# Kernel optimization log

Hardware: AMD Instinct MI355X
Metric: run time of the kernel (lower is better)

## Reference

```python
import jax, jax.numpy as jnp
import numpy as np

D_MODEL = 1024
N_HEADS = 16
D_K = D_MODEL // N_HEADS


def setup_inputs() -> dict:
    key = jax.random.key(0)
    ks = jax.random.split(key, 5)
    s = 1.0 / np.sqrt(D_MODEL)
    x = jax.random.normal(ks[0], (4, 2048, D_MODEL), dtype=jnp.float32)
    W_qkv = jax.random.normal(ks[1], (D_MODEL, 3 * D_MODEL), dtype=jnp.float32) * s
    b_qkv = jnp.zeros((3 * D_MODEL,), dtype=jnp.float32)
    W_proj = jax.random.normal(ks[2], (D_MODEL, D_MODEL), dtype=jnp.float32) * s
    b_proj = jnp.zeros((D_MODEL,), dtype=jnp.float32)
    return {"x": x, "W_qkv": W_qkv, "b_qkv": b_qkv, "W_proj": W_proj, "b_proj": b_proj}


def reference(x, W_qkv, b_qkv, W_proj, b_proj):
    B, T, C = x.shape
    qkv = x @ W_qkv + b_qkv  # [B,T,3C]
    q, k, v = jnp.split(qkv, 3, axis=2)
    # [B,T,C] -> [B,H,T,dk]
    def to_heads(t):
        return t.reshape(B, T, N_HEADS, D_K).transpose(0, 2, 1, 3)
    q, k, v = to_heads(q), to_heads(k), to_heads(v)
    scale = 1.0 / np.sqrt(D_K)
    att = jnp.einsum('bhqd,bhkd->bhqk', q, k) * scale
    causal = jnp.tril(jnp.ones((T, T), dtype=bool))
    att = jnp.where(causal, att, -jnp.inf)
    att = jax.nn.softmax(att, axis=-1)
    y = jnp.einsum('bhqk,bhkd->bhqd', att, v)
    y = y.transpose(0, 2, 1, 3).reshape(B, T, C)
    return y @ W_proj + b_proj
```

## Files before the change

### kernel.cpp

```cpp
#include <hip/hip_runtime.h>
#include <stdint.h>


typedef float  floatx4 __attribute__((ext_vector_type(4)));
typedef __bf16 bf16x8  __attribute__((ext_vector_type(8)));
typedef __bf16 bf16x4  __attribute__((ext_vector_type(4)));

#define AS1 __attribute__((address_space(1)))
#define AS3 __attribute__((address_space(3)))

__device__ __forceinline__ void gload_lds16(const void* g, void* l) {
    __builtin_amdgcn_global_load_lds((AS1 void*)(uintptr_t)g,
                                     (AS3 void*)(uintptr_t)l, 16, 0, 0);
}

#if __has_builtin(__builtin_amdgcn_exp2f)
#define EXP2F(x) __builtin_amdgcn_exp2f(x)
#else
#define EXP2F(x) exp2f(x)
#endif

#define LOG2E 1.44269504088896340736f
#define ATT_SC (0.125f * LOG2E)
#define MASK_NEG (-3.0e4f)

static constexpr int Bn = 4, Tn = 2048, Cn = 1024, Hn = 16, DKn = 64;
static constexpr int BT = Bn * Tn;
static constexpr int N_QKV = 3 * Cn;
static constexpr int PAD = 68;
static constexpr int VPAD = 132;


__global__ void cast_x_kernel(const float* __restrict__ x, __bf16* __restrict__ xb, int n) {
    int i = (blockIdx.x * blockDim.x + threadIdx.x) * 4;
    if (i < n) {
        float4 v = *(const float4*)(x + i);
        bf16x4 o;
        o[0] = (__bf16)v.x; o[1] = (__bf16)v.y; o[2] = (__bf16)v.z; o[3] = (__bf16)v.w;
        *(bf16x4*)(xb + i) = o;
    }
}

__global__ void transpose_cast_kernel(const float* __restrict__ W, __bf16* __restrict__ WT,
                                      int R, int C) {
    __shared__ float tile[32][33];
    int tx = threadIdx.x & 31, ty = threadIdx.x >> 5;
    int r0 = blockIdx.y * 32, c0 = blockIdx.x * 32;
#pragma unroll
    for (int i = 0; i < 4; i++)
        tile[ty + i * 8][tx] = W[(size_t)(r0 + ty + i * 8) * C + c0 + tx];
    __syncthreads();
#pragma unroll
    for (int i = 0; i < 4; i++)
        WT[(size_t)(c0 + ty + i * 8) * R + r0 + tx] = (__bf16)tile[tx][ty + i * 8];
}

__device__ __forceinline__ void xcd_swizzle(int gx, int* bn, int* bm) {
    int flat = blockIdx.y * gx + blockIdx.x;
    int nwg = gx * gridDim.y;
    int cpx = nwg >> 3;
    int swz = (flat & 7) * cpx + (flat >> 3);
    *bm = swz / gx;
    *bn = swz - *bm * gx;
}

__global__ __launch_bounds__(256) void gemm_qkv_kernel(
    const __bf16* __restrict__ A, const __bf16* __restrict__ Bt,
    const float* __restrict__ bias,
    __bf16* __restrict__ Qo, __bf16* __restrict__ Ko, __bf16* __restrict__ Vo) {
    const int K = 1024;
    __shared__ __bf16 Al[128 * 64];
    __shared__ __bf16 Bl[128 * 64];
    int tid = threadIdx.x, w = tid >> 6, lane = tid & 63;
    int lq = lane >> 4, l16 = lane & 15;
    int bm, bn;
    xcd_swizzle(gridDim.x, &bn, &bm);
    int wm = w & 1, wn = w >> 1;

    int srow = lane >> 3;
    int scb  = (lane & 7) ^ (srow & 7);
    const __bf16* Ag = A + (size_t)(bm * 128 + w * 32 + srow) * K + scb * 8;
    const __bf16* Bg = Bt + (size_t)(bn * 128 + w * 32 + srow) * K + scb * 8;
    __bf16* AlW = Al + w * 32 * 64;
    __bf16* BlW = Bl + w * 32 * 64;

    const int co0 = ((0 * 4 + lq) ^ (l16 & 7)) * 8;
    const int co1 = ((1 * 4 + lq) ^ (l16 & 7)) * 8;

    floatx4 acc[4][4] = {};
    for (int k0 = 0; k0 < K; k0 += 64) {
        __syncthreads();
#pragma unroll
        for (int c = 0; c < 4; c++) {
            gload_lds16(Ag + k0 + (size_t)c * 8 * K, AlW + c * 8 * 64);
            gload_lds16(Bg + k0 + (size_t)c * 8 * K, BlW + c * 8 * 64);
        }
        __syncthreads();
#pragma unroll
        for (int ks = 0; ks < 2; ks++) {
            const int co = ks ? co1 : co0;
            bf16x8 af[4], bf[4];
#pragma unroll
            for (int i = 0; i < 4; i++)
                af[i] = *(const bf16x8*)&Al[(wm * 64 + i * 16 + l16) * 64 + co];
#pragma unroll
            for (int i = 0; i < 4; i++)
                bf[i] = *(const bf16x8*)&Bl[(wn * 64 + i * 16 + l16) * 64 + co];
#pragma unroll
            for (int mt = 0; mt < 4; mt++)
#pragma unroll
                for (int nt = 0; nt < 4; nt++)
                    acc[mt][nt] = __builtin_amdgcn_mfma_f32_16x16x32_bf16(
                        af[mt], bf[nt], acc[mt][nt], 0, 0, 0);
        }
    }
#pragma unroll
    for (int nt = 0; nt < 4; nt++) {
        int gbase = bn * 128 + wn * 64 + nt * 16;
        int gcol = gbase + l16;
        int which = gbase >> 10;
        float bv = bias[gcol];
        if (which == 2) {
            int hh = (gbase - 2048) >> 6;
            int dd = ((gbase - 2048) & 63) + l16;
#pragma unroll
            for (int mt = 0; mt < 4; mt++) {
                int growb = bm * 128 + wm * 64 + mt * 16 + lq * 4;
                int bb = growb >> 11, tt = growb & 2047;
                bf16x4 v4;
#pragma unroll
                for (int r = 0; r < 4; r++) v4[r] = (__bf16)(acc[mt][nt][r] + bv);
                *(bf16x4*)&Vo[((size_t)(bb * 16 + hh) * 64 + dd) * 2048 + tt] = v4;
            }
        } else {
            int rem = gbase & 1023;
            int hh = rem >> 6, dd = (rem & 63) + l16;
            __bf16* dst = (which == 0) ? Qo : Ko;
            float scl = (which == 0) ? ATT_SC : 1.0f;
#pragma unroll
            for (int mt = 0; mt < 4; mt++) {
#pragma unroll
                for (int r = 0; r < 4; r++) {
                    int grow = bm * 128 + wm * 64 + mt * 16 + lq * 4 + r;
                    int bb = grow >> 11, tt = grow & 2047;
                    dst[((size_t)(bb * 16 + hh) * 2048 + tt) * 64 + dd] =
                        (__bf16)((acc[mt][nt][r] + bv) * scl);
                }
            }
        }
    }
}

__global__ __launch_bounds__(256) void gemm_proj_kernel(
    const __bf16* __restrict__ A, const __bf16* __restrict__ Bt,
    const float* __restrict__ bias, float* __restrict__ out) {
    const int K = 1024;
    __shared__ __bf16 Al[128 * 64];
    __shared__ __bf16 Bl[128 * 64];
    int tid = threadIdx.x, w = tid >> 6, lane = tid & 63;
    int lq = lane >> 4, l16 = lane & 15;
    int bm, bn;
    xcd_swizzle(gridDim.x, &bn, &bm);
    int wm = w & 1, wn = w >> 1;

    int srow = lane >> 3;
    int scb  = (lane & 7) ^ (srow & 7);
    const __bf16* Ag = A + (size_t)(bm * 128 + w * 32 + srow) * K + scb * 8;
    const __bf16* Bg = Bt + (size_t)(bn * 128 + w * 32 + srow) * K + scb * 8;
    __bf16* AlW = Al + w * 32 * 64;
    __bf16* BlW = Bl + w * 32 * 64;

    const int co0 = ((0 * 4 + lq) ^ (l16 & 7)) * 8;
    const int co1 = ((1 * 4 + lq) ^ (l16 & 7)) * 8;

    floatx4 acc[4][4] = {};
    for (int k0 = 0; k0 < K; k0 += 64) {
        __syncthreads();
#pragma unroll
        for (int c = 0; c < 4; c++) {
            gload_lds16(Ag + k0 + (size_t)c * 8 * K, AlW + c * 8 * 64);
            gload_lds16(Bg + k0 + (size_t)c * 8 * K, BlW + c * 8 * 64);
        }
        __syncthreads();
#pragma unroll
        for (int ks = 0; ks < 2; ks++) {
            const int co = ks ? co1 : co0;
            bf16x8 af[4], bf[4];
#pragma unroll
            for (int i = 0; i < 4; i++)
                af[i] = *(const bf16x8*)&Al[(wm * 64 + i * 16 + l16) * 64 + co];
#pragma unroll
            for (int i = 0; i < 4; i++)
                bf[i] = *(const bf16x8*)&Bl[(wn * 64 + i * 16 + l16) * 64 + co];
#pragma unroll
            for (int mt = 0; mt < 4; mt++)
#pragma unroll
                for (int nt = 0; nt < 4; nt++)
                    acc[mt][nt] = __builtin_amdgcn_mfma_f32_16x16x32_bf16(
                        af[mt], bf[nt], acc[mt][nt], 0, 0, 0);
        }
    }
#pragma unroll
    for (int nt = 0; nt < 4; nt++) {
        int gcol = bn * 128 + wn * 64 + nt * 16 + l16;
        float bv = bias[gcol];
#pragma unroll
        for (int mt = 0; mt < 4; mt++) {
#pragma unroll
            for (int r = 0; r < 4; r++) {
                int grow = bm * 128 + wm * 64 + mt * 16 + lq * 4 + r;
                out[(size_t)grow * 1024 + gcol] = acc[mt][nt][r] + bv;
            }
        }
    }
}

__global__ __launch_bounds__(256) void attn_kernel(
    const __bf16* __restrict__ Q, const __bf16* __restrict__ K,
    const __bf16* __restrict__ Vt, __bf16* __restrict__ Y) {
    const int bid = blockIdx.x;
    const int pr = bid >> 6, bh = bid & 63;
    const int b = bh >> 4, h = bh & 15;
    int tid = threadIdx.x, w = tid >> 6, lane = tid & 63;
    int lq = lane >> 4, l16 = lane & 15;

    const __bf16* Qh = Q + (size_t)bh * Tn * DKn;
    const __bf16* Kh = K + (size_t)bh * Tn * DKn;
    const __bf16* Vh = Vt + (size_t)bh * DKn * Tn;

    __shared__ __bf16 Kl[128 * PAD];
    __shared__ __bf16 Vl[64 * VPAD];
    __shared__ __bf16 Pl[128 * PAD];

    int skrow = tid >> 3, sksl = tid & 7;
    int svrow = tid >> 4, svsl = tid & 15;

    bf16x8 onesf;
#pragma unroll
    for (int j = 0; j < 8; j++) onesf[j] = (__bf16)1.0f;

    bf16x8 kr[4], vr[4];
#pragma unroll
    for (int i = 0; i < 4; i++) {
        kr[i] = *(const bf16x8*)&Kh[(size_t)(skrow + i * 32) * 64 + sksl * 8];
        vr[i] = *(const bf16x8*)&Vh[(size_t)(svrow + i * 16) * 2048 + svsl * 8];
    }

#pragma unroll
    for (int seg = 0; seg < 2; seg++) {
        const int qt = seg ? (15 - pr) : pr;
        const int q0 = qt * 128;
        const int ktmax = qt;

        bf16x8 qf[2][2];
#pragma unroll
        for (int mt = 0; mt < 2; mt++)
#pragma unroll
            for (int ks = 0; ks < 2; ks++)
                qf[mt][ks] = *(const bf16x8*)&Qh[(size_t)(q0 + w * 32 + mt * 16 + l16) * 64 +
                                                 ks * 32 + lq * 8];

        floatx4 oacc[2][5] = {};

        for (int kt = 0; kt <= ktmax; kt++) {
            __syncthreads();
#pragma unroll
            for (int i = 0; i < 4; i++) {
                *(bf16x8*)&Kl[(skrow + i * 32) * PAD + sksl * 8] = kr[i];
                *(bf16x8*)&Vl[(svrow + i * 16) * VPAD + svsl * 8] = vr[i];
            }
            __syncthreads();
            if (!(seg == 1 && kt == ktmax)) {
                int nk = (kt < ktmax) ? (kt + 1) : 0;
#pragma unroll
                for (int i = 0; i < 4; i++) {
                    kr[i] = *(const bf16x8*)&Kh[(size_t)(nk * 128 + skrow + i * 32) * 64 + sksl * 8];
                    vr[i] = *(const bf16x8*)&Vh[(size_t)(svrow + i * 16) * 2048 + nk * 128 + svsl * 8];
                }
            }

#pragma unroll
            for (int h2 = 0; h2 < 2; h2++) {
                floatx4 s2[2][4] = {};
#pragma unroll
                for (int ks = 0; ks < 2; ks++) {
                    bf16x8 kf[4];
#pragma unroll
                    for (int nt = 0; nt < 4; nt++)
                        kf[nt] = *(const bf16x8*)&Kl[(h2 * 64 + nt * 16 + l16) * PAD +
                                                     ks * 32 + lq * 8];
#pragma unroll
                    for (int mt = 0; mt < 2; mt++)
#pragma unroll
                        for (int nt = 0; nt < 4; nt++)
                            s2[mt][nt] = __builtin_amdgcn_mfma_f32_16x16x32_bf16(
                                qf[mt][ks], kf[nt], s2[mt][nt], 0, 0, 0);
                }

                if (kt == qt) {
#pragma unroll
                    for (int mt = 0; mt < 2; mt++)
#pragma unroll
                        for (int nt = 0; nt < 4; nt++) {
                            int col = kt * 128 + h2 * 64 + nt * 16 + l16;
#pragma unroll
                            for (int r = 0; r < 4; r++) {
                                int row = q0 + w * 32 + mt * 16 + lq * 4 + r;
                                if (col > row) s2[mt][nt][r] = MASK_NEG;
                            }
                        }
                }

#pragma unroll
                for (int mt = 0; mt < 2; mt++) {
#pragma unroll
                    for (int nt = 0; nt < 4; nt++) {
#pragma unroll
                        for (int r = 0; r < 4; r++) {
                            float p = EXP2F(s2[mt][nt][r]);
                            int rowl = w * 32 + mt * 16 + lq * 4 + r;
                            Pl[rowl * PAD + nt * 16 + l16] = (__bf16)p;
                        }
                    }
                }

#pragma unroll
                for (int ks = 0; ks < 2; ks++) {
                    bf16x8 pf[2], vf[4];
#pragma unroll
                    for (int mt = 0; mt < 2; mt++)
                        pf[mt] = *(const bf16x8*)&Pl[(w * 32 + mt * 16 + l16) * PAD +
                                                     ks * 32 + lq * 8];
#pragma unroll
                    for (int dt = 0; dt < 4; dt++)
                        vf[dt] = *(const bf16x8*)&Vl[(dt * 16 + l16) * VPAD +
                                                     h2 * 64 + ks * 32 + lq * 8];
#pragma unroll
                    for (int mt = 0; mt < 2; mt++) {
#pragma unroll
                        for (int dt = 0; dt < 4; dt++)
                            oacc[mt][dt] = __builtin_amdgcn_mfma_f32_16x16x32_bf16(
                                pf[mt], vf[dt], oacc[mt][dt], 0, 0, 0);
                        oacc[mt][4] = __builtin_amdgcn_mfma_f32_16x16x32_bf16(
                            pf[mt], onesf, oacc[mt][4], 0, 0, 0);
                    }
                }
            }
        }

#pragma unroll
        for (int mt = 0; mt < 2; mt++) {
#pragma unroll
            for (int r = 0; r < 4; r++) {
                float inv = 1.0f / oacc[mt][4][r];
                int rowg = q0 + w * 32 + mt * 16 + lq * 4 + r;
#pragma unroll
                for (int dt = 0; dt < 4; dt++)
                    Y[((size_t)(b * 2048 + rowg)) * 1024 + h * 64 + dt * 16 + l16] =
                        (__bf16)(oacc[mt][dt][r] * inv);
            }
        }
    }
}


extern "C" void kernel_launch(void* const* d_in, const int* in_sizes, int n_in,
                              void* d_out, int out_size, void* d_ws, size_t ws_size,
                              hipStream_t stream) {
    const float* x     = (const float*)d_in[0];
    const float* Wqkv  = (const float*)d_in[1];
    const float* bqkv  = (const float*)d_in[2];
    const float* Wproj = (const float*)d_in[3];
    const float* bproj = (const float*)d_in[4];
    float* out = (float*)d_out;

    __bf16* xb     = (__bf16*)d_ws;
    __bf16* WqkvT  = xb + (size_t)BT * Cn;
    __bf16* WprojT = WqkvT + (size_t)N_QKV * Cn;
    __bf16* Qb     = WprojT + (size_t)Cn * Cn;
    __bf16* Kb     = Qb + (size_t)BT * Cn;
    __bf16* Vb     = Kb + (size_t)BT * Cn;
    __bf16* Yb     = Vb + (size_t)BT * Cn;

    int nx = BT * Cn;
    cast_x_kernel<<<(nx / 4 + 255) / 256, 256, 0, stream>>>(x, xb, nx);
    transpose_cast_kernel<<<dim3(N_QKV / 32, Cn / 32), 256, 0, stream>>>(Wqkv, WqkvT, Cn, N_QKV);
    transpose_cast_kernel<<<dim3(Cn / 32, Cn / 32), 256, 0, stream>>>(Wproj, WprojT, Cn, Cn);

    gemm_qkv_kernel<<<dim3(N_QKV / 128, BT / 128), 256, 0, stream>>>(
        xb, WqkvT, bqkv, Qb, Kb, Vb);

    attn_kernel<<<dim3(512), 256, 0, stream>>>(Qb, Kb, Vb, Yb);

    gemm_proj_kernel<<<dim3(Cn / 128, BT / 128), 256, 0, stream>>>(
        Yb, WprojT, bproj, out);
}
```

Measured before the change: 246.9 us.

## Switch attention to 32x32 MFMA with register-resident P via bpermute

Rewrites the attention inner loop to use 32x32x16 bf16 MFMAs computing S^T (K as A operand, Q as B), so each lane holds one query column. The probabilities are packed to bf16 and rearranged across half-waves with ds_bpermute into the B-operand layout for the PV MFMA, which eliminates the shared-memory P buffer and its store/load round trip. LDS paddings are changed and output is written as 4-wide vectors. The risk is correctness of the lane permutation layout and different LDS bank-conflict behaviour from the new paddings.

```diff
diff --git a/kernel.cpp b/kernel.cpp
--- a/kernel.cpp
+++ b/kernel.cpp
@@ -2,9 +2,12 @@
 #include <stdint.h>
 
 
-typedef float  floatx4 __attribute__((ext_vector_type(4)));
-typedef __bf16 bf16x8  __attribute__((ext_vector_type(8)));
-typedef __bf16 bf16x4  __attribute__((ext_vector_type(4)));
+typedef float  floatx4  __attribute__((ext_vector_type(4)));
+typedef float  f32x16   __attribute__((ext_vector_type(16)));
+typedef __bf16 bf16x8   __attribute__((ext_vector_type(8)));
+typedef __bf16 bf16x4   __attribute__((ext_vector_type(4)));
+typedef unsigned int u32;
+typedef u32    u32x4    __attribute__((ext_vector_type(4)));
 
 #define AS1 __attribute__((address_space(1)))
 #define AS3 __attribute__((address_space(3)))
@@ -20,6 +23,12 @@
 #define EXP2F(x) exp2f(x)
 #endif
 
+__device__ __forceinline__ u32 pkbf(float lo, float hi) {
+    union { __bf16 h[2]; u32 u; } x;
+    x.h[0] = (__bf16)lo; x.h[1] = (__bf16)hi;
+    return x.u;
+}
+
 #define LOG2E 1.44269504088896340736f
 #define ATT_SC (0.125f * LOG2E)
 #define MASK_NEG (-3.0e4f)
@@ -27,8 +36,8 @@
 static constexpr int Bn = 4, Tn = 2048, Cn = 1024, Hn = 16, DKn = 64;
 static constexpr int BT = Bn * Tn;
 static constexpr int N_QKV = 3 * Cn;
-static constexpr int PAD = 68;
-static constexpr int VPAD = 132;
+static constexpr int KPAD = 66;
+static constexpr int VPAD = 130;
 
 
 __global__ void cast_x_kernel(const float* __restrict__ x, __bf16* __restrict__ xb, int n) {
@@ -222,15 +231,14 @@
     const int pr = bid >> 6, bh = bid & 63;
     const int b = bh >> 4, h = bh & 15;
     int tid = threadIdx.x, w = tid >> 6, lane = tid & 63;
-    int lq = lane >> 4, l16 = lane & 15;
+    int l32 = lane & 31, hi = lane >> 5;
 
     const __bf16* Qh = Q + (size_t)bh * Tn * DKn;
     const __bf16* Kh = K + (size_t)bh * Tn * DKn;
     const __bf16* Vh = Vt + (size_t)bh * DKn * Tn;
 
-    __shared__ __bf16 Kl[128 * PAD];
+    __shared__ __bf16 Kl[128 * KPAD];
     __shared__ __bf16 Vl[64 * VPAD];
-    __shared__ __bf16 Pl[128 * PAD];
 
     int skrow = tid >> 3, sksl = tid & 7;
     int svrow = tid >> 4, svsl = tid & 15;
@@ -238,6 +246,8 @@
     bf16x8 onesf;
 #pragma unroll
     for (int j = 0; j < 8; j++) onesf[j] = (__bf16)1.0f;
+
+    const int prt = (lane ^ 32) << 2;
 
     bf16x8 kr[4], vr[4];
 #pragma unroll
@@ -251,22 +261,20 @@
         const int qt = seg ? (15 - pr) : pr;
         const int q0 = qt * 128;
         const int ktmax = qt;
-
-        bf16x8 qf[2][2];
-#pragma unroll
-        for (int mt = 0; mt < 2; mt++)
-#pragma unroll
-            for (int ks = 0; ks < 2; ks++)
-                qf[mt][ks] = *(const bf16x8*)&Qh[(size_t)(q0 + w * 32 + mt * 16 + l16) * 64 +
-                                                 ks * 32 + lq * 8];
-
-        floatx4 oacc[2][5] = {};
+        const int qrow = q0 + w * 32 + l32;
+
+        bf16x8 qf[4];
+#pragma unroll
+        for (int ds = 0; ds < 4; ds++)
+            qf[ds] = *(const bf16x8*)&Qh[(size_t)qrow * 64 + ds * 16 + hi * 8];
+
+        f32x16 oacc0 = {}, oacc1 = {}, osum = {};
 
         for (int kt = 0; kt <= ktmax; kt++) {
             __syncthreads();
 #pragma unroll
             for (int i = 0; i < 4; i++) {
-                *(bf16x8*)&Kl[(skrow + i * 32) * PAD + sksl * 8] = kr[i];
+                *(bf16x8*)&Kl[(skrow + i * 32) * KPAD + sksl * 8] = kr[i];
                 *(bf16x8*)&Vl[(svrow + i * 16) * VPAD + svsl * 8] = vr[i];
             }
             __syncthreads();
@@ -280,84 +288,74 @@
             }
 
 #pragma unroll
-            for (int h2 = 0; h2 < 2; h2++) {
-                floatx4 s2[2][4] = {};
-#pragma unroll
-                for (int ks = 0; ks < 2; ks++) {
-                    bf16x8 kf[4];
-#pragma unroll
-                    for (int nt = 0; nt < 4; nt++)
-                        kf[nt] = *(const bf16x8*)&Kl[(h2 * 64 + nt * 16 + l16) * PAD +
-                                                     ks * 32 + lq * 8];
-#pragma unroll
-                    for (int mt = 0; mt < 2; mt++)
-#pragma unroll
-                        for (int nt = 0; nt < 4; nt++)
-                            s2[mt][nt] = __builtin_amdgcn_mfma_f32_16x16x32_bf16(
-                                qf[mt][ks], kf[nt], s2[mt][nt], 0, 0, 0);
+            for (int ktile = 0; ktile < 4; ktile++) {
+                f32x16 s = {};
+#pragma unroll
+                for (int ds = 0; ds < 4; ds++) {
+                    bf16x8 ka = *(const bf16x8*)&Kl[(ktile * 32 + l32) * KPAD +
+                                                    ds * 16 + hi * 8];
+                    s = __builtin_amdgcn_mfma_f32_32x32x16_bf16(ka, qf[ds], s, 0, 0, 0);
                 }
 
                 if (kt == qt) {
-#pragma unroll
-                    for (int mt = 0; mt < 2; mt++)
-#pragma unroll
-                        for (int nt = 0; nt < 4; nt++) {
-                            int col = kt * 128 + h2 * 64 + nt * 16 + l16;
-#pragma unroll
-                            for (int r = 0; r < 4; r++) {
-                                int row = q0 + w * 32 + mt * 16 + lq * 4 + r;
-                                if (col > row) s2[mt][nt][r] = MASK_NEG;
-                            }
-                        }
-                }
-
-#pragma unroll
-                for (int mt = 0; mt < 2; mt++) {
-#pragma unroll
-                    for (int nt = 0; nt < 4; nt++) {
-#pragma unroll
-                        for (int r = 0; r < 4; r++) {
-                            float p = EXP2F(s2[mt][nt][r]);
-                            int rowl = w * 32 + mt * 16 + lq * 4 + r;
-                            Pl[rowl * PAD + nt * 16 + l16] = (__bf16)p;
-                        }
+                    int kbase = kt * 128 + ktile * 32 + 4 * hi;
+#pragma unroll
+                    for (int r = 0; r < 16; r++) {
+                        int key = kbase + (r & 3) + 8 * (r >> 2);
+                        if (key > qrow) s[r] = MASK_NEG;
                     }
                 }
 
-#pragma unroll
-                for (int ks = 0; ks < 2; ks++) {
-                    bf16x8 pf[2], vf[4];
-#pragma unroll
-                    for (int mt = 0; mt < 2; mt++)
-                        pf[mt] = *(const bf16x8*)&Pl[(w * 32 + mt * 16 + l16) * PAD +
-                                                     ks * 32 + lq * 8];
-#pragma unroll
-                    for (int dt = 0; dt < 4; dt++)
-                        vf[dt] = *(const bf16x8*)&Vl[(dt * 16 + l16) * VPAD +
-                                                     h2 * 64 + ks * 32 + lq * 8];
-#pragma unroll
-                    for (int mt = 0; mt < 2; mt++) {
-#pragma unroll
-                        for (int dt = 0; dt < 4; dt++)
-                            oacc[mt][dt] = __builtin_amdgcn_mfma_f32_16x16x32_bf16(
-                                pf[mt], vf[dt], oacc[mt][dt], 0, 0, 0);
-                        oacc[mt][4] = __builtin_amdgcn_mfma_f32_16x16x32_bf16(
-                            pf[mt], onesf, oacc[mt][4], 0, 0, 0);
-                    }
-                }
-            }
-        }
-
-#pragma unroll
-        for (int mt = 0; mt < 2; mt++) {
-#pragma unroll
-            for (int r = 0; r < 4; r++) {
-                float inv = 1.0f / oacc[mt][4][r];
-                int rowg = q0 + w * 32 + mt * 16 + lq * 4 + r;
-#pragma unroll
-                for (int dt = 0; dt < 4; dt++)
-                    Y[((size_t)(b * 2048 + rowg)) * 1024 + h * 64 + dt * 16 + l16] =
-                        (__bf16)(oacc[mt][dt][r] * inv);
+                u32 G0a, G0b, G1a, G1b, G2a, G2b, G3a, G3b;
+                {
+                    float p0 = EXP2F(s[0]),  p1 = EXP2F(s[1]),  p2 = EXP2F(s[2]),  p3 = EXP2F(s[3]);
+                    float p4 = EXP2F(s[4]),  p5 = EXP2F(s[5]),  p6 = EXP2F(s[6]),  p7 = EXP2F(s[7]);
+                    float p8 = EXP2F(s[8]),  p9 = EXP2F(s[9]),  pa = EXP2F(s[10]), pb_ = EXP2F(s[11]);
+                    float pc = EXP2F(s[12]), pd = EXP2F(s[13]), pe = EXP2F(s[14]), pf = EXP2F(s[15]);
+                    G0a = pkbf(p0, p1);  G0b = pkbf(p2, p3);
+                    G1a = pkbf(p4, p5);  G1b = pkbf(p6, p7);
+                    G2a = pkbf(p8, p9);  G2b = pkbf(pa, pb_);
+                    G3a = pkbf(pc, pd);  G3b = pkbf(pe, pf);
+                }
+
+#pragma unroll
+                for (int t = 0; t < 2; t++) {
+                    u32 Ga0 = t ? G2a : G0a, Ga1 = t ? G2b : G0b;
+                    u32 Gb0 = t ? G3a : G1a, Gb1 = t ? G3b : G1b;
+                    u32 Z0 = hi ? Ga0 : Gb0;
+                    u32 Z1 = hi ? Ga1 : Gb1;
+                    u32 P0 = __builtin_amdgcn_ds_bpermute(prt, (int)Z0);
+                    u32 P1 = __builtin_amdgcn_ds_bpermute(prt, (int)Z1);
+                    u32 w0 = hi ? P0 : Ga0;
+                    u32 w1 = hi ? P1 : Ga1;
+                    u32 w2 = hi ? Gb0 : P0;
+                    u32 w3 = hi ? Gb1 : P1;
+                    u32x4 wv = {w0, w1, w2, w3};
+                    bf16x8 pbf = __builtin_bit_cast(bf16x8, wv);
+
+                    int kc = ktile * 32 + t * 16 + hi * 8;
+                    bf16x8 va0 = *(const bf16x8*)&Vl[(0 * 32 + l32) * VPAD + kc];
+                    bf16x8 va1 = *(const bf16x8*)&Vl[(1 * 32 + l32) * VPAD + kc];
+                    oacc0 = __builtin_amdgcn_mfma_f32_32x32x16_bf16(va0, pbf, oacc0, 0, 0, 0);
+                    oacc1 = __builtin_amdgcn_mfma_f32_32x32x16_bf16(va1, pbf, oacc1, 0, 0, 0);
+                    osum  = __builtin_amdgcn_mfma_f32_32x32x16_bf16(onesf, pbf, osum, 0, 0, 0);
+                }
+            }
+        }
+
+        float inv = 1.0f / osum[0];
+#pragma unroll
+        for (int dt2 = 0; dt2 < 2; dt2++) {
+#pragma unroll
+            for (int rg = 0; rg < 4; rg++) {
+                bf16x4 v4;
+#pragma unroll
+                for (int e = 0; e < 4; e++) {
+                    float o = dt2 ? oacc1[rg * 4 + e] : oacc0[rg * 4 + e];
+                    v4[e] = (__bf16)(o * inv);
+                }
+                int d = dt2 * 32 + 8 * rg + 4 * hi;
+                *(bf16x4*)&Y[((size_t)(b * 2048 + qrow)) * 1024 + h * 64 + d] = v4;
             }
         }
     }
```

Measured after the change: 254.1 us. 2.9% more time.
